# Kernel optimization log

Measured on AMD Instinct MI355X. Metric: run time of the kernel, lower is better.

The kernel has to match this reference:

```python
import jax, jax.numpy as jnp
import numpy as np

# init_kwargs baked as constants
GAMMA = 0.1
QTSE_WEIGHT = 1.0
SOFT_DTW_WEIGHT = 0.1
KQTSE = 0.1
BIG = 1e10  # finite stand-in for +inf so gradients stay NaN-free


def setup_inputs() -> dict:
    key = jax.random.key(0)
    k1, k2 = jax.random.split(key)
    predicted = jax.random.normal(k1, (32, 1024), dtype=jnp.float32)
    target = jax.random.normal(k2, (32, 1024), dtype=jnp.float32)
    return {"predicted": predicted, "target": target}


def _softmin3(a, b, c, gamma):
    # -gamma * log(exp(-a/g) + exp(-b/g) + exp(-c/g)), numerically stable
    z = jnp.stack([a, b, c]) * (-1.0 / gamma)
    return -gamma * jax.nn.logsumexp(z, axis=0)


def _soft_dtw(D, gamma):
    """Soft-DTW value per batch element.
    D: [B, N, M] pairwise squared distances. Returns [B].
    R[0,0]=0, R[i,0]=R[0,j]=inf; R[i,j] = D[i,j] + softmin(R[i-1,j-1], R[i-1,j], R[i,j-1]).
    Row-wise lax.scan (outer over i) with an inner scan over j carrying R[i,j-1].
    """
    B, N, M = D.shape
    big = jnp.asarray(BIG, D.dtype)
    # R[0, 0:M+1] = [0, inf, ..., inf]
    r0 = jnp.concatenate([jnp.zeros((B, 1), D.dtype),
                          jnp.full((B, M), big, D.dtype)], axis=1)  # [B, M+1]

    def row_step(r_prev, d_row):  # r_prev: [B, M+1] = R[i-1, :]; d_row: [M, B]
        r_diag = jnp.transpose(r_prev[:, :-1])  # [M, B] -> R[i-1, j-1]
        r_up = jnp.transpose(r_prev[:, 1:])     # [M, B] -> R[i-1, j]

        def col_step(r_left, inp):
            d, rd, ru = inp  # each [B]
            r = d + _softmin3(rd, ru, r_left, gamma)
            return r, r

        _, row = jax.lax.scan(col_step, jnp.full((B,), big, D.dtype),
                              (d_row, r_diag, r_up))  # row: [M, B] = R[i, 1:]
        r_new = jnp.concatenate([jnp.full((B, 1), big, D.dtype),
                                 jnp.transpose(row)], axis=1)  # [B, M+1]
        return r_new, None

    # xs over rows i=1..N: D rearranged to [N, M, B]
    r_final, _ = jax.lax.scan(row_step, r0, jnp.transpose(D, (1, 2, 0)))
    return r_final[:, -1]  # R[N, M] per batch element


def reference(predicted, target):
    # QTSE: quadratic loss with exponential asymmetry
    error = predicted - target
    qtse = jnp.mean(error ** 2 * jnp.exp(KQTSE * error))
    # soft-DTW between 1-d sequences: D[b,i,j] = (p_i - t_j)^2
    D = (predicted[:, :, None] - target[:, None, :]) ** 2  # [B, T, T]
    sdtw = jnp.mean(_soft_dtw(D, GAMMA))
    return SOFT_DTW_WEIGHT * sdtw + QTSE_WEIGHT * qtse
```

## Files before the change

kernel.cpp:

```cpp
#include <hip/hip_runtime.h>
#include <hip/hip_bf16.h>

#define BATCH 32
#define T 1024
#define WVS 8
#define NTH (WVS * 64)
#define KS 8
#define DOW 71
#define BIGF 1e10f
#define K2f 14.426950408889634f
#define GLN2f 0.0693147180559945f
#define KQTSE_ 0.1f

#define DG (BATCH * T)
#define OFF_AF 0
#define OFF_BF DG
#define OFF_AB (2 * DG)
#define OFF_BB (3 * DG)
#define SDTW_OFFF (4 * DG)
#define WS_NEEDED ((size_t)(4 * DG + 2 * BATCH) * 4)

__device__ __forceinline__ float fexp2(float x) {
    float r;
    asm("v_exp_f32 %0, %1" : "=v"(r) : "v"(x));
    return r;
}

__device__ __forceinline__ float softmin3(float a, float b, float c) {
    float m  = fminf(fminf(a, b), c);
    float M  = fmaxf(fmaxf(a, b), c);
    float md = __builtin_amdgcn_fmed3f(a, b, c);
    float mk = m * K2f;
    float e1 = fexp2(fmaf(-K2f, md, mk));
    float e2 = fexp2(fmaf(-K2f, M, mk));
    return fmaf(-GLN2f, __log2f(1.0f + e1 + e2), m);
}

__device__ __forceinline__ float lane_shr1(float old, float src) {
    return __int_as_float(__builtin_amdgcn_update_dpp(
        __float_as_int(old), __float_as_int(src), 0x138, 0xF, 0xF, false));
}

__global__ __launch_bounds__(NTH) void sdtw_half(const float* __restrict__ pred,
                                                 const float* __restrict__ targ,
                                                 float* __restrict__ ws) {
    __shared__ float p[T];
    __shared__ float ring[WVS - 1][T];

    const int blk = blockIdx.x;
    const int b = blk & (BATCH - 1);
    const int dir = blk >> 5;
    const int tid = threadIdx.x;
    const int wv = tid >> 6;
    const int ln = tid & 63;
    const int myoff = DOW * wv + ln;

    const float2 pv2 = ((const float2*)(pred + b * T))[tid];
    if (dir == 0) {
        ((float2*)p)[tid] = pv2;
    } else {
        p[T - 1 - 2 * tid] = pv2.x;
        p[T - 2 - 2 * tid] = pv2.y;
    }
    const int c0g = dir ? (T - 1 - 2 * tid) : (2 * tid);
    const int c1g = dir ? (T - 2 - 2 * tid) : (2 * tid + 1);
    const float tj0 = targ[b * T + c0g];
    const float tj1 = targ[b * T + c1g];
    const float zcc = (tid == 0) ? 0.0f : BIGF;

    const int q = (dir ? 1023 : 1021) - 2 * tid;
    const int nb = 128 + dir;

    float top0 = BIGF, top1 = BIGF, corner = BIGF, rc = BIGF;
    float rA0 = BIGF, rB0 = BIGF, rA1 = BIGF, rB1 = BIGF;

    __syncthreads();

    for (int sb = 0; sb < nb; ++sb) {
        const int ics = sb * KS - myoff;

        float rl[KS];
#pragma unroll
        for (int so = 0; so < KS; ++so) rl[so] = BIGF;
        if (ln == 0 && wv > 0) {
#pragma unroll
            for (int so = 0; so < KS; ++so) rl[so] = ring[wv - 1][(ics + so) & (T - 1)];
        }

        float Dv0[KS], Dv1[KS];
#pragma unroll
        for (int so = 0; so < KS; ++so) {
            const float pr = p[(ics + so) & (T - 1)];
            const float d0 = pr - tj0;
            const float d1 = pr - tj1;
            Dv0[so] = d0 * d0;
            Dv1[so] = d1 * d1;
        }

#pragma unroll
        for (int so = 0; so < KS; ++so) {
            const int ic = ics + so;
            const float lf = lane_shr1(rl[so], rc);
            const bool r0 = (ic == 0);
            const float t0 = r0 ? BIGF : top0;
            const float t1 = r0 ? BIGF : top1;
            const float cc = r0 ? zcc : corner;

            const float c00 = Dv0[so] + softmin3(cc, t0, lf);
            const float c01 = Dv1[so] + softmin3(t0, t1, c00);

            if (ic == q - 1) rA1 = c01;
            if (ic == q)     { rA0 = c00; rB1 = c01; }
            if (ic == q + 1) rB0 = c00;

            rc = c01; top0 = c00; top1 = c01; corner = lf;
            if (ln == 63 && wv < WVS - 1 && (unsigned)ic < (unsigned)T)
                ring[wv][ic] = c01;
        }
        __syncthreads();
    }

    float* dgA = ws + (dir ? OFF_AB : OFF_AF) + b * T;
    float* dgB = ws + (dir ? OFF_BB : OFF_BF) + b * T;
    dgA[2 * tid] = rA0;
    dgA[2 * tid + 1] = rA1;
    dgB[2 * tid] = rB0;
    dgB[2 * tid + 1] = rB1;
}

__global__ __launch_bounds__(1024) void merge_kernel(const float* __restrict__ pred,
                                                     const float* __restrict__ targ,
                                                     float* __restrict__ ws) {
    const int b = blockIdx.x;
    const int tid = threadIdx.x;
    const float* dgAf = ws + OFF_AF + b * T;
    const float* dgBf = ws + OFF_BF + b * T;
    const float* dgAb = ws + OFF_AB + b * T;
    const float* dgBb = ws + OFF_BB + b * T;

    float t1 = BIGF, t2 = BIGF;
    if (tid >= 1) {
        const float d = pred[b * T + tid - 1] - targ[b * T + 1023 - tid];
        t1 = dgBf[1023 - tid] + dgBb[tid] - d * d;
    }
    if (tid >= 1 && tid <= 1022) {
        t2 = dgAf[1022 - tid] + dgAb[tid];
    }
    const float e = pred[b * T + tid] - targ[b * T + tid];
    float qacc = e * e * __expf(KQTSE_ * e);

    __shared__ float red[16];
    __shared__ float redq[16];
    __shared__ float bcast;
    const int wv = tid >> 6, ln = tid & 63;

    float mn = fminf(t1, t2);
    for (int off = 32; off; off >>= 1) mn = fminf(mn, __shfl_xor(mn, off, 64));
    if (ln == 0) red[wv] = mn;
    __syncthreads();
    if (tid == 0) {
        float m = red[0];
        for (int w = 1; w < 16; ++w) m = fminf(m, red[w]);
        bcast = m;
    }
    __syncthreads();
    const float m = bcast;

    float s = fexp2((m - t1) * K2f) + fexp2((m - t2) * K2f);
    for (int off = 32; off; off >>= 1) s += __shfl_xor(s, off, 64);
    for (int off = 32; off; off >>= 1) qacc += __shfl_xor(qacc, off, 64);
    __syncthreads();
    if (ln == 0) { red[wv] = s; redq[wv] = qacc; }
    __syncthreads();
    if (tid == 0) {
        float tot = 0.0f, qt = 0.0f;
        for (int w = 0; w < 16; ++w) { tot += red[w]; qt += redq[w]; }
        ws[SDTW_OFFF + b] = fmaf(-GLN2f, __log2f(tot), m);
        ws[SDTW_OFFF + BATCH + b] = qt;
    }
}

__global__ __launch_bounds__(64) void finish_small(const float* __restrict__ sd,
                                                   float* __restrict__ out) {
    const int l = threadIdx.x;
    float s = (l < BATCH) ? sd[l] : 0.0f;
    float qv = (l < BATCH) ? sd[BATCH + l] : 0.0f;
    for (int off = 32; off; off >>= 1) {
        s += __shfl_down(s, off, 64);
        qv += __shfl_down(qv, off, 64);
    }
    if (l == 0) out[0] = 0.1f * (s / (float)BATCH) + qv / (float)(BATCH * T);
}

#define FB_KS 16
#define FB_DOW 79
#define FB_NB 83

__global__ __launch_bounds__(256) void sdtw_fb(const float* __restrict__ pred,
                                               const float* __restrict__ targ,
                                               float* __restrict__ sdtw_out) {
    __shared__ float p[T];
    __shared__ float ring[3][T];
    const int b = blockIdx.x;
    const int tid = threadIdx.x;
    const int wv = tid >> 6, ln = tid & 63;
    const int myoff = FB_DOW * wv + ln;
    ((float4*)p)[tid] = ((const float4*)(pred + b * T))[tid];
    const float4 t4 = ((const float4*)(targ + b * T))[tid];
    const float tj0 = t4.x, tj1 = t4.y, tj2 = t4.z, tj3 = t4.w;
    const float zcc = (tid == 0) ? 0.0f : BIGF;
    float top0 = BIGF, top1 = BIGF, top2 = BIGF, top3 = BIGF;
    float corner = BIGF, rc = BIGF, result = 0.0f;
    __syncthreads();
    for (int sb = 0; sb < FB_NB; ++sb) {
        const int ics = sb * FB_KS - myoff;
        float rl[FB_KS];
#pragma unroll
        for (int so = 0; so < FB_KS; ++so) rl[so] = BIGF;
        if (ln == 0 && wv > 0) {
#pragma unroll
            for (int so = 0; so < FB_KS; ++so) rl[so] = ring[wv - 1][(ics + so) & (T - 1)];
        }
        float Dv0[FB_KS], Dv1[FB_KS], Dv2[FB_KS], Dv3[FB_KS];
#pragma unroll
        for (int so = 0; so < FB_KS; ++so) {
            const float pr = p[(ics + so) & (T - 1)];
            const float d0 = pr - tj0, d1 = pr - tj1, d2 = pr - tj2, d3 = pr - tj3;
            Dv0[so] = d0 * d0; Dv1[so] = d1 * d1; Dv2[so] = d2 * d2; Dv3[so] = d3 * d3;
        }
#pragma unroll
        for (int so = 0; so < FB_KS; ++so) {
            const int ic = ics + so;
            const float lf = lane_shr1(rl[so], rc);
            const bool r0 = (ic == 0);
            const float t0 = r0 ? BIGF : top0;
            const float t1 = r0 ? BIGF : top1;
            const float t2 = r0 ? BIGF : top2;
            const float t3 = r0 ? BIGF : top3;
            const float cc = r0 ? zcc : corner;
            const float c0 = Dv0[so] + softmin3(cc, t0, lf);
            const float c1 = Dv1[so] + softmin3(t0, t1, c0);
            const float c2 = Dv2[so] + softmin3(t1, t2, c1);
            const float c3 = Dv3[so] + softmin3(t2, t3, c2);
            rc = c3; top0 = c0; top1 = c1; top2 = c2; top3 = c3;
            corner = lf;
            if ((unsigned)ic < (unsigned)T) result = c3;
            if (ln == 63 && wv < 3 && (unsigned)ic < (unsigned)T) ring[wv][ic] = c3;
        }
        __syncthreads();
    }
    if (tid == 255) sdtw_out[b] = result;
}

__global__ __launch_bounds__(1024) void finish_kernel(const float* __restrict__ pred,
                                                      const float* __restrict__ targ,
                                                      const float* __restrict__ sdtw,
                                                      float* __restrict__ out) {
    const int tid = threadIdx.x;
    float acc = 0.0f;
    for (int idx = tid; idx < BATCH * T; idx += 1024) {
        const float e = pred[idx] - targ[idx];
        acc += e * e * __expf(KQTSE_ * e);
    }
    for (int off = 32; off; off >>= 1) acc += __shfl_down(acc, off, 64);
    __shared__ float red[16];
    const int wave = tid >> 6, lane = tid & 63;
    if (lane == 0) red[wave] = acc;
    __syncthreads();
    if (tid == 0) {
        float qv = 0.0f;
        for (int w = 0; w < 16; ++w) qv += red[w];
        qv /= (float)(BATCH * T);
        float s = 0.0f;
        for (int bb = 0; bb < BATCH; ++bb) s += sdtw[bb];
        s /= (float)BATCH;
        out[0] = 0.1f * s + 1.0f * qv;
    }
}

extern "C" void kernel_launch(void* const* d_in, const int* in_sizes, int n_in,
                              void* d_out, int out_size, void* d_ws, size_t ws_size,
                              hipStream_t stream) {
    const float* pred = (const float*)d_in[0];
    const float* targ = (const float*)d_in[1];
    float* out = (float*)d_out;

    if (ws_size >= WS_NEEDED) {
        float* ws = (float*)d_ws;
        sdtw_half<<<BATCH * 2, NTH, 0, stream>>>(pred, targ, ws);
        merge_kernel<<<BATCH, 1024, 0, stream>>>(pred, targ, ws);
        finish_small<<<1, 64, 0, stream>>>(ws + SDTW_OFFF, out);
    } else {
        float* sdtw = (float*)d_ws;
        sdtw_fb<<<BATCH, 256, 0, stream>>>(pred, targ, sdtw);
        finish_kernel<<<1, 1024, 0, stream>>>(pred, targ, sdtw, out);
    }
}
```

Baseline: 192.2 us.

## Skip idle wavefront steps and interleave wave ranks across SIMDs

Each wavefront now only runs the wavefront-sweep body during the superblocks where its anti-diagonal band overlaps the half-matrix, skipping the dead ramp-up and drain iterations. Waves are also remapped to a logical rank order (0,2,4,6,7,5,3,1) so that waves active at the same time are spread across SIMDs rather than clustered. This is meant to cut issue slots wasted on idle cells and to balance SIMD load. The barrier each superblock is kept, so the critical path length is unchanged.

```diff
diff --git a/kernel.cpp b/kernel.cpp
--- a/kernel.cpp
+++ b/kernel.cpp
@@ -53,7 +53,9 @@
     const int tid = threadIdx.x;
     const int wv = tid >> 6;
     const int ln = tid & 63;
-    const int myoff = DOW * wv + ln;
+    const int rank = (wv < 4) ? (2 * wv) : (15 - 2 * wv);
+    const int vtid = (rank << 6) + ln;
+    const int myoff = DOW * rank + ln;
 
     const float2 pv2 = ((const float2*)(pred + b * T))[tid];
     if (dir == 0) {
@@ -62,14 +64,16 @@
         p[T - 1 - 2 * tid] = pv2.x;
         p[T - 2 - 2 * tid] = pv2.y;
     }
-    const int c0g = dir ? (T - 1 - 2 * tid) : (2 * tid);
-    const int c1g = dir ? (T - 2 - 2 * tid) : (2 * tid + 1);
+    const int c0g = dir ? (T - 1 - 2 * vtid) : (2 * vtid);
+    const int c1g = dir ? (T - 2 - 2 * vtid) : (2 * vtid + 1);
     const float tj0 = targ[b * T + c0g];
     const float tj1 = targ[b * T + c1g];
-    const float zcc = (tid == 0) ? 0.0f : BIGF;
-
-    const int q = (dir ? 1023 : 1021) - 2 * tid;
+    const float zcc = (vtid == 0) ? 0.0f : BIGF;
+
+    const int q = (dir ? 1023 : 1021) - 2 * vtid;
     const int nb = 128 + dir;
+    const int wA = (DOW * rank) >> 3;
+    const int wB = (1022 + 2 * dir - 57 * rank) >> 3;
 
     float top0 = BIGF, top1 = BIGF, corner = BIGF, rc = BIGF;
     float rA0 = BIGF, rB0 = BIGF, rA1 = BIGF, rB1 = BIGF;
@@ -77,55 +81,57 @@
     __syncthreads();
 
     for (int sb = 0; sb < nb; ++sb) {
-        const int ics = sb * KS - myoff;
-
-        float rl[KS];
-#pragma unroll
-        for (int so = 0; so < KS; ++so) rl[so] = BIGF;
-        if (ln == 0 && wv > 0) {
-#pragma unroll
-            for (int so = 0; so < KS; ++so) rl[so] = ring[wv - 1][(ics + so) & (T - 1)];
-        }
-
-        float Dv0[KS], Dv1[KS];
-#pragma unroll
-        for (int so = 0; so < KS; ++so) {
-            const float pr = p[(ics + so) & (T - 1)];
-            const float d0 = pr - tj0;
-            const float d1 = pr - tj1;
-            Dv0[so] = d0 * d0;
-            Dv1[so] = d1 * d1;
-        }
-
-#pragma unroll
-        for (int so = 0; so < KS; ++so) {
-            const int ic = ics + so;
-            const float lf = lane_shr1(rl[so], rc);
-            const bool r0 = (ic == 0);
-            const float t0 = r0 ? BIGF : top0;
-            const float t1 = r0 ? BIGF : top1;
-            const float cc = r0 ? zcc : corner;
-
-            const float c00 = Dv0[so] + softmin3(cc, t0, lf);
-            const float c01 = Dv1[so] + softmin3(t0, t1, c00);
-
-            if (ic == q - 1) rA1 = c01;
-            if (ic == q)     { rA0 = c00; rB1 = c01; }
-            if (ic == q + 1) rB0 = c00;
-
-            rc = c01; top0 = c00; top1 = c01; corner = lf;
-            if (ln == 63 && wv < WVS - 1 && (unsigned)ic < (unsigned)T)
-                ring[wv][ic] = c01;
+        if (sb >= wA && sb <= wB) {
+            const int ics = sb * KS - myoff;
+
+            float rl[KS];
+#pragma unroll
+            for (int so = 0; so < KS; ++so) rl[so] = BIGF;
+            if (ln == 0 && rank > 0) {
+#pragma unroll
+                for (int so = 0; so < KS; ++so) rl[so] = ring[rank - 1][(ics + so) & (T - 1)];
+            }
+
+            float Dv0[KS], Dv1[KS];
+#pragma unroll
+            for (int so = 0; so < KS; ++so) {
+                const float pr = p[(ics + so) & (T - 1)];
+                const float d0 = pr - tj0;
+                const float d1 = pr - tj1;
+                Dv0[so] = d0 * d0;
+                Dv1[so] = d1 * d1;
+            }
+
+#pragma unroll
+            for (int so = 0; so < KS; ++so) {
+                const int ic = ics + so;
+                const float lf = lane_shr1(rl[so], rc);
+                const bool r0 = (ic == 0);
+                const float t0 = r0 ? BIGF : top0;
+                const float t1 = r0 ? BIGF : top1;
+                const float cc = r0 ? zcc : corner;
+
+                const float c00 = Dv0[so] + softmin3(cc, t0, lf);
+                const float c01 = Dv1[so] + softmin3(t0, t1, c00);
+
+                if (ic == q - 1) rA1 = c01;
+                if (ic == q)     { rA0 = c00; rB1 = c01; }
+                if (ic == q + 1) rB0 = c00;
+
+                rc = c01; top0 = c00; top1 = c01; corner = lf;
+                if (ln == 63 && rank < WVS - 1 && (unsigned)ic < (unsigned)T)
+                    ring[rank][ic] = c01;
+            }
         }
         __syncthreads();
     }
 
     float* dgA = ws + (dir ? OFF_AB : OFF_AF) + b * T;
     float* dgB = ws + (dir ? OFF_BB : OFF_BF) + b * T;
-    dgA[2 * tid] = rA0;
-    dgA[2 * tid + 1] = rA1;
-    dgB[2 * tid] = rB0;
-    dgB[2 * tid + 1] = rB1;
+    dgA[2 * vtid] = rA0;
+    dgA[2 * vtid + 1] = rA1;
+    dgB[2 * vtid] = rB0;
+    dgB[2 * vtid + 1] = rB1;
 }
 
 __global__ __launch_bounds__(1024) void merge_kernel(const float* __restrict__ pred,
```

Measured after the change: 172.6 us. 1.11x faster.
